# Performance work log

Measured on AMD Instinct MI355X. Metric: run time of the kernel, lower is better.

The kernel has to match this reference:

```python
import jax, jax.numpy as jnp
import numpy as np

NUM_ITER = 5
ALPHA = 5.0   # spatial bandwidth, bilateral kernel
BETA = 5.0    # feature bandwidth, bilateral kernel
GAMMA = 5.0   # spatial bandwidth, spatial kernel
W_1 = 1.0
W_2 = 1.0


def setup_inputs() -> dict:
    key = jax.random.key(0)
    k1, k2 = jax.random.split(key)
    B, C, X, Y, Z = 1, 4, 32, 16, 16
    log_unary = jax.random.normal(k1, (B, C, X, Y, Z), dtype=jnp.float32)
    features_pairwise = jax.random.normal(k2, (B, 2, X, Y, Z), dtype=jnp.float32)
    # Potts-model compatibility: ones minus identity, [C_out, C_in] (conv1d kernel size 1)
    compatibility_weights = (jnp.ones((C, C)) - jnp.eye(C)).astype(jnp.float32)
    return {"log_unary": log_unary, "features_pairwise": features_pairwise,
            "compatibility_weights": compatibility_weights}


def _gauss_kernel(f):
    # f: [B, D, N] feature vectors; dense Gaussian filter matrix K_ij = exp(-||f_i-f_j||^2/2)
    sq = jnp.sum(f * f, axis=1)  # [B, N]
    d2 = sq[:, :, None] + sq[:, None, :] - 2.0 * jnp.einsum('bdn,bdm->bnm', f, f)
    return jnp.exp(-0.5 * jnp.maximum(d2, 0.0))  # [B, N, N]


def reference(log_unary, features_pairwise, compatibility_weights):
    B, C, X, Y, Z = log_unary.shape
    N = X * Y * Z
    lu = log_unary.reshape(B, C, N)
    q = jax.nn.softmax(lu, axis=1)

    gx, gy, gz = jnp.meshgrid(jnp.arange(X), jnp.arange(Y), jnp.arange(Z), indexing='ij')
    spatial = jnp.stack([gx, gy, gz], axis=0).astype(jnp.float32).reshape(1, 3, N)
    spatial = jnp.broadcast_to(spatial, (B, 3, N))
    img_fea = features_pairwise.reshape(B, features_pairwise.shape[1], N)

    f1 = jnp.concatenate([spatial / ALPHA, img_fea / BETA], axis=1)  # bilateral features
    f2 = spatial / GAMMA                                             # spatial features

    K1 = _gauss_kernel(f1)
    K2 = _gauss_kernel(f2)
    # norm = filter(ones) = row sums; scale = rsqrt(norm)
    scale1 = jax.lax.rsqrt(jnp.sum(K1, axis=2))[:, None, :]  # [B,1,N]
    scale2 = jax.lax.rsqrt(jnp.sum(K2, axis=2))[:, None, :]

    for _ in range(NUM_ITER):
        q1 = jnp.einsum('bnm,bcm->bcn', K1, q * scale1) * scale1
        q2 = jnp.einsum('bnm,bcm->bcn', K2, q * scale2) * scale2
        q_comb = W_1 * q1 + W_2 * q2
        q_update = jnp.einsum('oc,bcn->bon', compatibility_weights, q_comb)
        q = jax.nn.softmax(lu - q_update, axis=1)

    return q.reshape(B, C, X, Y, Z)
```

## Files before the change

kernel.cpp:

```cpp
#include <hip/hip_runtime.h>
#include <math.h>


constexpr int   NT    = 8192;
constexpr float LOG2E = 1.4426950408889634f;
constexpr float SQL2E = 1.2011224087864498f;
constexpr float INVA  = 0.2f * SQL2E;

constexpr int R_M = 0, R_U1 = 32, R_U2 = 36, R_S1 = 40, R_S2 = 41, R_CV = 42;

static __device__ __forceinline__ float ex2(float x) {
    return __builtin_amdgcn_exp2f(x);
}

__constant__ float INVSQF[7] = {1.f, 1.f, 0.70710678f, 0.40824829f,
                                0.20412415f, 0.09128709f, 0.03726780f};
__constant__ int AB_A[28] = {0, 1,0, 2,1,0, 3,2,1,0, 4,3,2,1,0,
                             5,4,3,2,1,0, 6,5,4,3,2,1,0};
__constant__ int AB_B[28] = {0, 0,1, 0,1,2, 0,1,2,3, 0,1,2,3,4,
                             0,1,2,3,4,5, 0,1,2,3,4,5,6};

static __device__ __forceinline__ void conv3d_store512(float* SP,
                                                       float* __restrict__ outp,
                                                       const float* w0,
                                                       const float* w1,
                                                       int tid) {
    float g32[32];
#pragma unroll
    for (int d = 0; d < 32; d++) { float t = d * INVA; g32[d] = ex2(-0.5f*t*t); }
    __syncthreads();
    {
        int r = tid;
        float v[16], acc[16];
#pragma unroll
        for (int z = 0; z < 16; z++) { v[z] = SP[r*17 + z]; acc[z] = 0.f; }
#pragma unroll
        for (int zp = 0; zp < 16; zp++)
#pragma unroll
            for (int z = 0; z < 16; z++) {
                int d = (z > zp) ? (z - zp) : (zp - z);
                acc[z] = fmaf(g32[d], v[zp], acc[z]);
            }
#pragma unroll
        for (int z = 0; z < 16; z++) SP[r*17 + z] = acc[z];
    }
    __syncthreads();
    {
        int x = tid >> 4, z = tid & 15;
        int base = x * 272 + z;
        float v[16], acc[16];
#pragma unroll
        for (int y = 0; y < 16; y++) { v[y] = SP[base + y*17]; acc[y] = 0.f; }
#pragma unroll
        for (int yp = 0; yp < 16; yp++)
#pragma unroll
            for (int y = 0; y < 16; y++) {
                int d = (y > yp) ? (y - yp) : (yp - y);
                acc[y] = fmaf(g32[d], v[yp], acc[y]);
            }
#pragma unroll
        for (int y = 0; y < 16; y++) SP[base + y*17] = acc[y];
    }
    __syncthreads();
    {
        int c = tid & 255, h = tid >> 8;
        int base = (c >> 4) * 17 + (c & 15);
        float v[32];
#pragma unroll
        for (int xp = 0; xp < 32; xp++) v[xp] = SP[base + xp*272];
        float acc[16];
#pragma unroll
        for (int x0 = 0; x0 < 16; x0++) acc[x0] = 0.f;
        if (h == 0) {
#pragma unroll
            for (int xp = 0; xp < 32; xp++)
#pragma unroll
                for (int x0 = 0; x0 < 16; x0++) {
                    int d = (x0 > xp) ? (x0 - xp) : (xp - x0);
                    acc[x0] = fmaf(g32[d], v[xp], acc[x0]);
                }
#pragma unroll
            for (int x0 = 0; x0 < 16; x0++) {
                int n = x0*256 + c;
                float w = w0 ? w0[n] : 1.f;
                if (w1) w *= w1[n];
                outp[n] = w * acc[x0];
            }
        } else {
#pragma unroll
            for (int xp = 0; xp < 32; xp++)
#pragma unroll
                for (int x0 = 0; x0 < 16; x0++) {
                    int x = x0 + 16;
                    int d = (x > xp) ? (x - xp) : (xp - x);
                    acc[x0] = fmaf(g32[d], v[xp], acc[x0]);
                }
#pragma unroll
            for (int x0 = 0; x0 < 16; x0++) {
                int n = (x0+16)*256 + c;
                float w = w0 ? w0[n] : 1.f;
                if (w1) w *= w1[n];
                outp[n] = w * acc[x0];
            }
        }
    }
}

__global__ __launch_bounds__(512) void k_phaseA(const float* __restrict__ feat,
                                                float* __restrict__ W) {
    __shared__ float SP[512 * 17];
    const int bid = blockIdx.x, tid = threadIdx.x;
    if (bid < 28) {
        const int a = AB_A[bid], b = AB_B[bid];
        const float ca = INVSQF[a], cb = INVSQF[b];
        for (int s = tid; s < NT; s += 512) {
            float g0 = feat[s] * 0.2f, g1 = feat[NT + s] * 0.2f;
            float eg = ex2(-0.5f * LOG2E * (g0*g0 + g1*g1));
            float pa = 1.f;
            for (int i = 0; i < a; i++) pa *= g0;
            float pb = 1.f;
            for (int i = 0; i < b; i++) pb *= g1;
            float v = eg * pa * ca * pb * cb;
            W[(R_M + bid)*NT + s] = v;
            SP[(s >> 4)*17 + (s & 15)] = v;
        }
        conv3d_store512(SP, W + (R_CV + bid)*NT, W + (R_M + bid)*NT, nullptr, tid);
    } else {
#pragma unroll
        for (int i = 0; i < 4; i++) {
            int n = (bid - 28) * 2048 + i*512 + tid;
            int x = n >> 8, y = (n >> 4) & 15, z = n & 15;
            float Sx = 0.f, Sy = 0.f, Sz = 0.f;
            for (int j = 0; j < 32; j++) { float d = (float)(x-j)*INVA; Sx += ex2(-0.5f*d*d); }
            for (int j = 0; j < 16; j++) { float d = (float)(y-j)*INVA; Sy += ex2(-0.5f*d*d); }
            for (int j = 0; j < 16; j++) { float d = (float)(z-j)*INVA; Sz += ex2(-0.5f*d*d); }
            W[R_S2*NT + n] = rsqrtf(Sx * Sy * Sz);
        }
    }
}

__global__ __launch_bounds__(256) void k_init(float* __restrict__ W,
                                              const float* __restrict__ lu) {
    int n = blockIdx.x * 256 + threadIdx.x;
    float rs = 0.f;
#pragma unroll
    for (int ab = 0; ab < 28; ab++)
        rs += W[(R_CV+ab)*NT + n];
    float s1 = rsqrtf(rs);
    float s2 = W[R_S2*NT + n];
    W[R_S1*NT + n] = s1;
    float l0 = lu[n], l1 = lu[NT+n], l2 = lu[2*NT+n], l3 = lu[3*NT+n];
    float mx = fmaxf(fmaxf(l0,l1), fmaxf(l2,l3));
    float q0 = __expf(l0-mx), q1 = __expf(l1-mx), q2 = __expf(l2-mx), q3 = __expf(l3-mx);
    float inv = 1.f / (q0+q1+q2+q3);
    q0*=inv; q1*=inv; q2*=inv; q3*=inv;
    W[(R_U1+0)*NT+n]=q0*s1; W[(R_U1+1)*NT+n]=q1*s1; W[(R_U1+2)*NT+n]=q2*s1; W[(R_U1+3)*NT+n]=q3*s1;
    W[(R_U2+0)*NT+n]=q0*s2; W[(R_U2+1)*NT+n]=q1*s2; W[(R_U2+2)*NT+n]=q2*s2; W[(R_U2+3)*NT+n]=q3*s2;
}

__global__ __launch_bounds__(512) void k_conv(const float* __restrict__ W,
                                              float* __restrict__ Wout) {
    __shared__ float SP[512 * 17];
    const int idx = blockIdx.x;
    const int tid = threadIdx.x;
    if (idx < 112) {
        const float4* M4 = (const float4*)(W + (R_M + (idx >> 2))*NT);
        const float4* U4 = (const float4*)(W + (R_U1 + (idx & 3))*NT);
#pragma unroll
        for (int i = 0; i < 4; i++) {
            int s4 = tid + i*512;
            float4 m = M4[s4], u = U4[s4];
            int s = s4 << 2;
            int base = (s >> 4)*17 + (s & 15);
            SP[base+0] = m.x*u.x; SP[base+1] = m.y*u.y;
            SP[base+2] = m.z*u.z; SP[base+3] = m.w*u.w;
        }
        conv3d_store512(SP, Wout + (R_CV + idx)*NT,
                        W + (R_M + (idx >> 2))*NT, W + R_S1*NT, tid);
    } else {
        const float4* U4 = (const float4*)(W + (R_U2 + (idx - 112))*NT);
#pragma unroll
        for (int i = 0; i < 4; i++) {
            int s4 = tid + i*512;
            float4 u = U4[s4];
            int s = s4 << 2;
            int base = (s >> 4)*17 + (s & 15);
            SP[base+0] = u.x; SP[base+1] = u.y; SP[base+2] = u.z; SP[base+3] = u.w;
        }
        conv3d_store512(SP, Wout + (R_CV + idx)*NT, W + R_S2*NT, nullptr, tid);
    }
}

__global__ __launch_bounds__(256) void k_fuse(float* __restrict__ W,
        const float* __restrict__ lu, const float* __restrict__ compat,
        float* __restrict__ out, int last) {
    int n = blockIdx.x * 256 + threadIdx.x;
    float comb[4] = {0.f, 0.f, 0.f, 0.f};
#pragma unroll
    for (int ab = 0; ab < 28; ab++)
#pragma unroll
        for (int c = 0; c < 4; c++)
            comb[c] += W[(R_CV + ab*4 + c)*NT + n];
#pragma unroll
    for (int c = 0; c < 4; c++)
        comb[c] += W[(R_CV + 112 + c)*NT + n];
    float q[4];
#pragma unroll
    for (int o = 0; o < 4; o++) {
        float upd = 0.f;
#pragma unroll
        for (int c = 0; c < 4; c++) upd = fmaf(compat[o*4+c], comb[c], upd);
        q[o] = lu[o*NT+n] - upd;
    }
    float mx = fmaxf(fmaxf(q[0],q[1]), fmaxf(q[2],q[3]));
    float sum = 0.f;
#pragma unroll
    for (int c = 0; c < 4; c++) { q[c] = __expf(q[c]-mx); sum += q[c]; }
    float inv = 1.f / sum;
    if (last) {
#pragma unroll
        for (int c = 0; c < 4; c++) out[c*NT+n] = q[c] * inv;
    } else {
        float s1 = W[R_S1*NT + n], s2 = W[R_S2*NT + n];
#pragma unroll
        for (int c = 0; c < 4; c++) {
            float qq = q[c] * inv;
            W[(R_U1+c)*NT+n] = qq*s1;
            W[(R_U2+c)*NT+n] = qq*s2;
        }
    }
}

extern "C" void kernel_launch(void* const* d_in, const int* in_sizes, int n_in,
                              void* d_out, int out_size, void* d_ws, size_t ws_size,
                              hipStream_t stream) {
    const float* lu     = (const float*)d_in[0];
    const float* feat   = (const float*)d_in[1];
    const float* compat = (const float*)d_in[2];
    float* out = (float*)d_out;
    float* W   = (float*)d_ws;

    k_phaseA<<<dim3(32),  dim3(512), 0, stream>>>(feat, W);
    k_init  <<<dim3(32),  dim3(256), 0, stream>>>(W, lu);
    for (int it = 0; it < 5; it++) {
        k_conv<<<dim3(116), dim3(512), 0, stream>>>(W, W);
        k_fuse<<<dim3(32),  dim3(256), 0, stream>>>(W, lu, compat, out, it == 4);
    }
}
```

Before: 131.1 us.

## Fuse softmax update into conv kernel and reduce conv outputs with atomics

After: 176.5 us. +34.7%, slower.

```diff
diff --git a/kernel.cpp b/kernel.cpp
--- a/kernel.cpp
+++ b/kernel.cpp
@@ -8,6 +8,7 @@
 constexpr float INVA  = 0.2f * SQL2E;
 
 constexpr int R_M = 0, R_U1 = 32, R_U2 = 36, R_S1 = 40, R_S2 = 41, R_CV = 42;
+constexpr int R_CB = 70;
 
 static __device__ __forceinline__ float ex2(float x) {
     return __builtin_amdgcn_exp2f(x);
@@ -20,11 +21,12 @@
 __constant__ int AB_B[28] = {0, 0,1, 0,1,2, 0,1,2,3, 0,1,2,3,4,
                              0,1,2,3,4,5, 0,1,2,3,4,5,6};
 
-static __device__ __forceinline__ void conv3d_store512(float* SP,
-                                                       float* __restrict__ outp,
-                                                       const float* w0,
-                                                       const float* w1,
-                                                       int tid) {
+template <int ATOMIC>
+static __device__ __forceinline__ void conv3d_out512(float* SP,
+                                                     float* __restrict__ outp,
+                                                     const float* w0,
+                                                     const float* w1,
+                                                     int tid) {
     float g32[32];
 #pragma unroll
     for (int d = 0; d < 32; d++) { float t = d * INVA; g32[d] = ex2(-0.5f*t*t); }
@@ -84,7 +86,8 @@
                 int n = x0*256 + c;
                 float w = w0 ? w0[n] : 1.f;
                 if (w1) w *= w1[n];
-                outp[n] = w * acc[x0];
+                if (ATOMIC) unsafeAtomicAdd(&outp[n], w * acc[x0]);
+                else        outp[n] = w * acc[x0];
             }
         } else {
 #pragma unroll
@@ -100,7 +103,8 @@
                 int n = (x0+16)*256 + c;
                 float w = w0 ? w0[n] : 1.f;
                 if (w1) w *= w1[n];
-                outp[n] = w * acc[x0];
+                if (ATOMIC) unsafeAtomicAdd(&outp[n], w * acc[x0]);
+                else        outp[n] = w * acc[x0];
             }
         }
     }
@@ -124,7 +128,7 @@
             W[(R_M + bid)*NT + s] = v;
             SP[(s >> 4)*17 + (s & 15)] = v;
         }
-        conv3d_store512(SP, W + (R_CV + bid)*NT, W + (R_M + bid)*NT, nullptr, tid);
+        conv3d_out512<0>(SP, W + (R_CV + bid)*NT, W + (R_M + bid)*NT, nullptr, tid);
     } else {
 #pragma unroll
         for (int i = 0; i < 4; i++) {
@@ -156,60 +160,94 @@
     q0*=inv; q1*=inv; q2*=inv; q3*=inv;
     W[(R_U1+0)*NT+n]=q0*s1; W[(R_U1+1)*NT+n]=q1*s1; W[(R_U1+2)*NT+n]=q2*s1; W[(R_U1+3)*NT+n]=q3*s1;
     W[(R_U2+0)*NT+n]=q0*s2; W[(R_U2+1)*NT+n]=q1*s2; W[(R_U2+2)*NT+n]=q2*s2; W[(R_U2+3)*NT+n]=q3*s2;
-}
-
-__global__ __launch_bounds__(512) void k_conv(const float* __restrict__ W,
-                                              float* __restrict__ Wout) {
+#pragma unroll
+    for (int k = 0; k < 20; k++) W[(R_CB + k)*NT + n] = 0.f;
+}
+
+__global__ __launch_bounds__(512) void k_conv(float* __restrict__ W,
+        const float* __restrict__ lu, const float* __restrict__ compat, int it) {
     __shared__ float SP[512 * 17];
     const int idx = blockIdx.x;
     const int tid = threadIdx.x;
-    if (idx < 112) {
-        const float4* M4 = (const float4*)(W + (R_M + (idx >> 2))*NT);
-        const float4* U4 = (const float4*)(W + (R_U1 + (idx & 3))*NT);
-#pragma unroll
-        for (int i = 0; i < 4; i++) {
-            int s4 = tid + i*512;
-            float4 m = M4[s4], u = U4[s4];
-            int s = s4 << 2;
-            int base = (s >> 4)*17 + (s & 15);
-            SP[base+0] = m.x*u.x; SP[base+1] = m.y*u.y;
-            SP[base+2] = m.z*u.z; SP[base+3] = m.w*u.w;
-        }
-        conv3d_store512(SP, Wout + (R_CV + idx)*NT,
-                        W + (R_M + (idx >> 2))*NT, W + R_S1*NT, tid);
+    const bool spat = (idx >= 112);
+    const int ch = spat ? (idx - 112) : (idx & 3);
+
+    if (it == 0) {
+        if (!spat) {
+            const float4* M4 = (const float4*)(W + (R_M + (idx >> 2))*NT);
+            const float4* U4 = (const float4*)(W + (R_U1 + ch)*NT);
+#pragma unroll
+            for (int i = 0; i < 4; i++) {
+                int s4 = tid + i*512;
+                float4 m = M4[s4], u = U4[s4];
+                int s = s4 << 2;
+                int base = (s >> 4)*17 + (s & 15);
+                SP[base+0] = m.x*u.x; SP[base+1] = m.y*u.y;
+                SP[base+2] = m.z*u.z; SP[base+3] = m.w*u.w;
+            }
+        } else {
+            const float4* U4 = (const float4*)(W + (R_U2 + ch)*NT);
+#pragma unroll
+            for (int i = 0; i < 4; i++) {
+                int s4 = tid + i*512;
+                float4 u = U4[s4];
+                int s = s4 << 2;
+                int base = (s >> 4)*17 + (s & 15);
+                SP[base+0] = u.x; SP[base+1] = u.y; SP[base+2] = u.z; SP[base+3] = u.w;
+            }
+        }
     } else {
-        const float4* U4 = (const float4*)(W + (R_U2 + (idx - 112))*NT);
-#pragma unroll
-        for (int i = 0; i < 4; i++) {
-            int s4 = tid + i*512;
-            float4 u = U4[s4];
-            int s = s4 << 2;
-            int base = (s >> 4)*17 + (s & 15);
-            SP[base+0] = u.x; SP[base+1] = u.y; SP[base+2] = u.z; SP[base+3] = u.w;
-        }
-        conv3d_store512(SP, Wout + (R_CV + idx)*NT, W + R_S2*NT, nullptr, tid);
-    }
-}
-
-__global__ __launch_bounds__(256) void k_fuse(float* __restrict__ W,
+        const float* cb = W + (R_CB + (it-1)*4)*NT;
+        const float* srow = spat ? (W + R_S2*NT) : (W + R_S1*NT);
+        const float* Mr = W + (R_M + (idx >> 2))*NT;
+        float cmp[16];
+#pragma unroll
+        for (int i = 0; i < 16; i++) cmp[i] = compat[i];
+#pragma unroll
+        for (int i = 0; i < 16; i++) {
+            int s = tid + i*512;
+            float c0 = cb[s],      c1 = cb[NT+s],
+                  c2 = cb[2*NT+s], c3 = cb[3*NT+s];
+            float q[4];
+#pragma unroll
+            for (int o = 0; o < 4; o++) {
+                float upd = 0.f;
+                upd = fmaf(cmp[o*4+0], c0, upd);
+                upd = fmaf(cmp[o*4+1], c1, upd);
+                upd = fmaf(cmp[o*4+2], c2, upd);
+                upd = fmaf(cmp[o*4+3], c3, upd);
+                q[o] = lu[o*NT+s] - upd;
+            }
+            float mx = fmaxf(fmaxf(q[0],q[1]), fmaxf(q[2],q[3]));
+            float sum = 0.f;
+#pragma unroll
+            for (int c = 0; c < 4; c++) { q[c] = __expf(q[c]-mx); sum += q[c]; }
+            float qc = (ch==0) ? q[0] : (ch==1) ? q[1] : (ch==2) ? q[2] : q[3];
+            float u = (qc / sum) * srow[s];
+            SP[(s >> 4)*17 + (s & 15)] = spat ? u : (Mr[s] * u);
+        }
+    }
+    float* combp = W + (R_CB + it*4 + ch)*NT;
+    if (!spat)
+        conv3d_out512<1>(SP, combp, W + (R_M + (idx >> 2))*NT, W + R_S1*NT, tid);
+    else
+        conv3d_out512<1>(SP, combp, W + R_S2*NT, nullptr, tid);
+}
+
+__global__ __launch_bounds__(256) void k_out(const float* __restrict__ W,
         const float* __restrict__ lu, const float* __restrict__ compat,
-        float* __restrict__ out, int last) {
+        float* __restrict__ out) {
     int n = blockIdx.x * 256 + threadIdx.x;
-    float comb[4] = {0.f, 0.f, 0.f, 0.f};
-#pragma unroll
-    for (int ab = 0; ab < 28; ab++)
-#pragma unroll
-        for (int c = 0; c < 4; c++)
-            comb[c] += W[(R_CV + ab*4 + c)*NT + n];
-#pragma unroll
-    for (int c = 0; c < 4; c++)
-        comb[c] += W[(R_CV + 112 + c)*NT + n];
+    const float* cb = W + (R_CB + 16)*NT;
+    float c0 = cb[n], c1 = cb[NT+n], c2 = cb[2*NT+n], c3 = cb[3*NT+n];
     float q[4];
 #pragma unroll
     for (int o = 0; o < 4; o++) {
         float upd = 0.f;
-#pragma unroll
-        for (int c = 0; c < 4; c++) upd = fmaf(compat[o*4+c], comb[c], upd);
+        upd = fmaf(compat[o*4+0], c0, upd);
+        upd = fmaf(compat[o*4+1], c1, upd);
+        upd = fmaf(compat[o*4+2], c2, upd);
+        upd = fmaf(compat[o*4+3], c3, upd);
         q[o] = lu[o*NT+n] - upd;
     }
     float mx = fmaxf(fmaxf(q[0],q[1]), fmaxf(q[2],q[3]));
@@ -217,18 +255,8 @@
 #pragma unroll
     for (int c = 0; c < 4; c++) { q[c] = __expf(q[c]-mx); sum += q[c]; }
     float inv = 1.f / sum;
-    if (last) {
-#pragma unroll
-        for (int c = 0; c < 4; c++) out[c*NT+n] = q[c] * inv;
-    } else {
-        float s1 = W[R_S1*NT + n], s2 = W[R_S2*NT + n];
-#pragma unroll
-        for (int c = 0; c < 4; c++) {
-            float qq = q[c] * inv;
-            W[(R_U1+c)*NT+n] = qq*s1;
-            W[(R_U2+c)*NT+n] = qq*s2;
-        }
-    }
+#pragma unroll
+    for (int c = 0; c < 4; c++) out[c*NT+n] = q[c] * inv;
 }
 
 extern "C" void kernel_launch(void* const* d_in, const int* in_sizes, int n_in,
@@ -242,8 +270,7 @@
 
     k_phaseA<<<dim3(32),  dim3(512), 0, stream>>>(feat, W);
     k_init  <<<dim3(32),  dim3(256), 0, stream>>>(W, lu);
-    for (int it = 0; it < 5; it++) {
-        k_conv<<<dim3(116), dim3(512), 0, stream>>>(W, W);
-        k_fuse<<<dim3(32),  dim3(256), 0, stream>>>(W, lu, compat, out, it == 4);
-    }
-}
+    for (int it = 0; it < 5; it++)
+        k_conv<<<dim3(116), dim3(512), 0, stream>>>(W, lu, compat, it);
+    k_out   <<<dim3(32),  dim3(256), 0, stream>>>(W, lu, compat, out);
+}
```
